# Performance work log

Hardware: AMD Instinct MI355X
Metric: run time of the kernel (lower is better)

Reference implementation:

```python
import jax, jax.numpy as jnp
import numpy as np

N_POINTS = 1_000_000
# Voigt index pairs (11,22,33,12,13,23)
_II = jnp.array([0, 1, 2, 0, 0, 1])
_JJ = jnp.array([0, 1, 2, 1, 2, 2])


def _P_of(F, c1, c2):
    """First Piola-Kirchhoff stress of compressible Neo-Hookean psi."""
    FinvT = jnp.linalg.inv(F).T
    I1 = jnp.trace(F.T @ F)
    J = jnp.linalg.det(F)
    Jm23 = jnp.power(J, -2.0 / 3.0)
    return 2.0 * c1 * Jm23 * (F - (I1 / 3.0) * FinvT) + 2.0 * c2 * (J - 1.0) * J * FinvT


def _per_point(F, c1, c2):
    I1 = jnp.trace(F.T @ F)
    J = jnp.linalg.det(F)
    Jm23 = jnp.power(J, -2.0 / 3.0)
    psi = c1 * (Jm23 * I1 - 3.0) + c2 * (J - 1.0) ** 2

    P = _P_of(F, c1, c2)                      # (3,3)
    P_F = jax.jacfwd(_P_of)(F, c1, c2)        # (3,3,3,3) = d P_ij / d F_kl

    Kirchhoff = P @ F.T                       # tau = P F^T
    Cauchy = Kirchhoff / J
    EYE = jnp.eye(3, dtype=F.dtype)

    # push-forward of the material tangent + geometric correction
    Stiff = jnp.einsum('iqks,jq,ls->ijkl', P_F, F, F)
    Stiff = Stiff + 0.5 * (
        jnp.einsum('ik,jl->ijkl', Kirchhoff, EYE)
        + jnp.einsum('il,jk->ijkl', Kirchhoff, EYE)
        + jnp.einsum('jk,il->ijkl', Kirchhoff, EYE)
        - jnp.einsum('jl,ik->ijkl', Kirchhoff, EYE)
    )

    Cauchy6 = Cauchy[_II, _JJ]                                            # (6,)
    DDSDDE = Stiff[_II[:, None], _JJ[:, None], _II[None, :], _JJ[None, :]] / J  # (6,6)
    return psi, Cauchy6, DDSDDE


def setup_inputs() -> dict:
    key = jax.random.key(0)
    k1, k2 = jax.random.split(key)
    # near-identity deformation gradients (positive det, small strain)
    noise = jax.random.normal(k1, (N_POINTS, 3, 3), dtype=jnp.float32)
    F_in = jnp.eye(3, dtype=jnp.float32)[None] + 0.05 * noise
    mat_par = 0.5 + jax.random.uniform(k2, (2,), dtype=jnp.float32)  # (c1, c2) > 0
    return {"F_in": F_in, "mat_par": mat_par}


def reference(F_in, mat_par):
    c1, c2 = mat_par[0], mat_par[1]
    psi, Cauchy6, DDSDDE = jax.vmap(_per_point, in_axes=(0, None, None))(F_in, c1, c2)
    return psi, Cauchy6, DDSDDE
```

## Files before the change

kernel.cpp:

```cpp
#include <hip/hip_runtime.h>

static constexpr int VII[6] = {0, 1, 2, 0, 0, 1};
static constexpr int VJJ[6] = {0, 1, 2, 1, 2, 2};

__device__ __forceinline__ void nh_compute(const float F[3][3], float c1, float c2,
                                           float& psi, float cau[6], float dd[36])
{
    const float J = F[0][0] * (F[1][1] * F[2][2] - F[1][2] * F[2][1])
                  - F[0][1] * (F[1][0] * F[2][2] - F[1][2] * F[2][0])
                  + F[0][2] * (F[1][0] * F[2][1] - F[1][1] * F[2][0]);

    float b[3][3];
#pragma unroll
    for (int r = 0; r < 3; ++r)
#pragma unroll
        for (int c = 0; c < 3; ++c) {
            if (c > r) continue;
            const float s = F[r][0] * F[c][0] + F[r][1] * F[c][1] + F[r][2] * F[c][2];
            b[r][c] = s;
            b[c][r] = s;
        }

    const float I1   = b[0][0] + b[1][1] + b[2][2];
    const float invJ = 1.0f / J;
    const float Jm23 = cbrtf(invJ * invJ);

    psi = c1 * (Jm23 * I1 - 3.0f) + c2 * (J - 1.0f) * (J - 1.0f);

    const float c1t  = 2.0f * c1 * Jm23;
    const float diag = 2.0f * c2 * (J - 1.0f) * J - c1t * (I1 * (1.0f / 3.0f));
    float tau[3][3];
#pragma unroll
    for (int r = 0; r < 3; ++r)
#pragma unroll
        for (int c = 0; c < 3; ++c)
            tau[r][c] = c1t * b[r][c] + (r == c ? diag : 0.0f);

#pragma unroll
    for (int a = 0; a < 6; ++a)
        cau[a] = tau[VII[a]][VJJ[a]] * invJ;

    const float gE  = 2.0f * c2 * (2.0f * J - 1.0f) * J;
    const float gF  = -2.0f * c2 * (J - 1.0f) * J;
    const float cA  = c1t * (2.0f * I1 * (1.0f / 9.0f));
    const float cB  = c1t * (I1 * (1.0f / 3.0f));
    const float m23 = -(2.0f / 3.0f) * c1t;

#pragma unroll
    for (int a = 0; a < 6; ++a) {
        const int i = VII[a], j = VJJ[a];
#pragma unroll
        for (int q = 0; q < 6; ++q) {
            const int k = VII[q], l = VJJ[q];
            float s = 0.0f;
            if (i == k) s += c1t * b[j][l];
            if (k == l) s += m23 * b[i][j];
            if (i == j) s += m23 * b[k][l];
            if (i == j && k == l) s += cA + gE;
            if (i == l && j == k) s += cB + gF;
            float g = 0.0f;
            if (j == l) g += tau[i][k];
            if (j == k) g += tau[i][l];
            if (i == l) g += tau[j][k];
            if (i == k) g -= tau[j][l];
            dd[6 * a + q] = (s + 0.5f * g) * invJ;
        }
    }
}

#define WPB 4
#define DPAD 37

__global__ __launch_bounds__(256) void nh3d_coal(
    const float* __restrict__ Fg, const float* __restrict__ mp,
    float* __restrict__ out, int N, int nWaves)
{
    __shared__ float sbuf[WPB][64 * DPAD];

    const int tid  = threadIdx.x;
    const int wave = tid >> 6;
    const int lane = tid & 63;
    const int waveIdx = blockIdx.x * WPB + wave;
    if (waveIdx >= nWaves) return;
    const int waveStart = waveIdx * 64;
    const int idx = waveStart + lane;

    const float c1 = mp[0];
    const float c2 = mp[1];

    float F[3][3];
    {
        const float* fp = Fg + (size_t)idx * 9;
#pragma unroll
        for (int r = 0; r < 3; ++r)
#pragma unroll
            for (int c = 0; c < 3; ++c)
                F[r][c] = fp[3 * r + c];
    }

    float psi, cau[6], dd[36];
    nh_compute(F, c1, c2, psi, cau, dd);

    out[idx] = psi;

    float* sw = sbuf[wave];

#pragma unroll
    for (int j = 0; j < 36; ++j)
        sw[lane * DPAD + j] = dd[j];

    float* dout = out + (size_t)7 * N + (size_t)waveStart * 36;
#pragma unroll
    for (int k = 0; k < 9; ++k) {
        const int g = k * 256 + lane * 4;
        const int p = g / 36;
        const int base = p * DPAD + (g - p * 36);
        const float4 v = make_float4(sw[base], sw[base + 1], sw[base + 2], sw[base + 3]);
        *reinterpret_cast<float4*>(dout + g) = v;
    }

#pragma unroll
    for (int j = 0; j < 6; ++j)
        sw[lane * 7 + j] = cau[j];

    float* cout_ = out + (size_t)N + (size_t)waveStart * 6;
#pragma unroll
    for (int k = 0; k < 3; ++k) {
        const int g = k * 128 + lane * 2;
        const int p = g / 6;
        const int base = p * 7 + (g - p * 6);
        *reinterpret_cast<float2*>(cout_ + g) = make_float2(sw[base], sw[base + 1]);
    }
}

__global__ __launch_bounds__(256) void nh3d_scatter(
    const float* __restrict__ Fg, const float* __restrict__ mp,
    float* __restrict__ out, int N, int start)
{
    const int idx = start + blockIdx.x * blockDim.x + threadIdx.x;
    if (idx >= N) return;

    const float c1 = mp[0];
    const float c2 = mp[1];

    float F[3][3];
    {
        const float* fp = Fg + (size_t)idx * 9;
#pragma unroll
        for (int r = 0; r < 3; ++r)
#pragma unroll
            for (int c = 0; c < 3; ++c)
                F[r][c] = fp[3 * r + c];
    }

    float psi, cau[6], dd[36];
    nh_compute(F, c1, c2, psi, cau, dd);

    out[idx] = psi;
    float* cout_ = out + (size_t)N + (size_t)idx * 6;
    float* dout  = out + (size_t)7 * N + (size_t)idx * 36;
#pragma unroll
    for (int a = 0; a < 6; ++a) cout_[a] = cau[a];
#pragma unroll
    for (int a = 0; a < 36; ++a) dout[a] = dd[a];
}

extern "C" void kernel_launch(void* const* d_in, const int* in_sizes, int n_in,
                              void* d_out, int out_size, void* d_ws, size_t ws_size,
                              hipStream_t stream) {
    const int N = in_sizes[0] / 9;
    const float* F_in    = (const float*)d_in[0];
    const float* mat_par = (const float*)d_in[1];
    float* out = (float*)d_out;

    if (N >= 64 && (N % 4) == 0) {
        const int nWaves = N / 64;
        const int grid = (nWaves + WPB - 1) / WPB;
        nh3d_coal<<<grid, 256, 0, stream>>>(F_in, mat_par, out, N, nWaves);
        const int tail = N - nWaves * 64;
        if (tail > 0) {
            nh3d_scatter<<<1, 64, 0, stream>>>(F_in, mat_par, out, N, nWaves * 64);
        }
    } else {
        const int grid = (N + 255) / 256;
        nh3d_scatter<<<grid, 256, 0, stream>>>(F_in, mat_par, out, N, 0);
    }
}
```

Before: 194.0 us.

## Stage input through LDS, use vector LDS layout, nontemporal stores, fast math

The F input is loaded with coalesced float4 reads into LDS per wave and then read back per lane, replacing strided 9-float loads. The output staging now uses an unpadded float4 LDS layout, writes go out as nontemporal vector stores, and the symmetric DDSDDE matrix is computed only for its upper triangle and mirrored. J^-2/3 and 1/J use hardware log/exp2/rcp intrinsics in the fast path. The unpadded float4 LDS layout may cause bank conflicts, and the approximate intrinsics slightly change numerics.

```diff
diff --git a/kernel.cpp b/kernel.cpp
--- a/kernel.cpp
+++ b/kernel.cpp
@@ -1,8 +1,14 @@
 #include <hip/hip_runtime.h>
+
+typedef float f32x4 __attribute__((ext_vector_type(4)));
+typedef float f32x2 __attribute__((ext_vector_type(2)));
+
+#define LDS_FENCE() asm volatile("" ::: "memory")
 
 static constexpr int VII[6] = {0, 1, 2, 0, 0, 1};
 static constexpr int VJJ[6] = {0, 1, 2, 1, 2, 2};
 
+template <bool FAST>
 __device__ __forceinline__ void nh_compute(const float F[3][3], float c1, float c2,
                                            float& psi, float cau[6], float dd[36])
 {
@@ -14,16 +20,21 @@
 #pragma unroll
     for (int r = 0; r < 3; ++r)
 #pragma unroll
-        for (int c = 0; c < 3; ++c) {
-            if (c > r) continue;
+        for (int c = 0; c <= r; ++c) {
             const float s = F[r][0] * F[c][0] + F[r][1] * F[c][1] + F[r][2] * F[c][2];
             b[r][c] = s;
             b[c][r] = s;
         }
 
-    const float I1   = b[0][0] + b[1][1] + b[2][2];
-    const float invJ = 1.0f / J;
-    const float Jm23 = cbrtf(invJ * invJ);
+    const float I1 = b[0][0] + b[1][1] + b[2][2];
+    float invJ, Jm23;
+    if (FAST) {
+        invJ = __builtin_amdgcn_rcpf(J);
+        Jm23 = __builtin_amdgcn_exp2f(-(2.0f / 3.0f) * __builtin_amdgcn_logf(J));
+    } else {
+        invJ = 1.0f / J;
+        Jm23 = cbrtf(invJ * invJ);
+    }
 
     psi = c1 * (Jm23 * I1 - 3.0f) + c2 * (J - 1.0f) * (J - 1.0f);
 
@@ -50,7 +61,7 @@
     for (int a = 0; a < 6; ++a) {
         const int i = VII[a], j = VJJ[a];
 #pragma unroll
-        for (int q = 0; q < 6; ++q) {
+        for (int q = a; q < 6; ++q) {
             const int k = VII[q], l = VJJ[q];
             float s = 0.0f;
             if (i == k) s += c1t * b[j][l];
@@ -63,19 +74,20 @@
             if (j == k) g += tau[i][l];
             if (i == l) g += tau[j][k];
             if (i == k) g -= tau[j][l];
-            dd[6 * a + q] = (s + 0.5f * g) * invJ;
+            const float v = (s + 0.5f * g) * invJ;
+            dd[6 * a + q] = v;
+            if (q != a) dd[6 * q + a] = v;
         }
     }
 }
 
 #define WPB 4
-#define DPAD 37
 
 __global__ __launch_bounds__(256) void nh3d_coal(
     const float* __restrict__ Fg, const float* __restrict__ mp,
     float* __restrict__ out, int N, int nWaves)
 {
-    __shared__ float sbuf[WPB][64 * DPAD];
+    __shared__ f32x4 sbuf[WPB][576];
 
     const int tid  = threadIdx.x;
     const int wave = tid >> 6;
@@ -83,53 +95,59 @@
     const int waveIdx = blockIdx.x * WPB + wave;
     if (waveIdx >= nWaves) return;
     const int waveStart = waveIdx * 64;
-    const int idx = waveStart + lane;
 
     const float c1 = mp[0];
     const float c2 = mp[1];
 
+    f32x4* sv = sbuf[wave];
+    const float* sf = reinterpret_cast<const float*>(sv);
+
+    {
+        const f32x4* gin = reinterpret_cast<const f32x4*>(Fg + (size_t)waveStart * 9);
+        sv[lane]      = gin[lane];
+        sv[64 + lane] = gin[64 + lane];
+        if (lane < 16) sv[128 + lane] = gin[128 + lane];
+    }
+    LDS_FENCE();
     float F[3][3];
+#pragma unroll
+    for (int r = 0; r < 3; ++r)
+#pragma unroll
+        for (int c = 0; c < 3; ++c)
+            F[r][c] = sf[lane * 9 + 3 * r + c];
+    LDS_FENCE();
+
+    float psi, cau[6], dd[36];
+    nh_compute<true>(F, c1, c2, psi, cau, dd);
+
+    __builtin_nontemporal_store(psi, out + waveStart + lane);
+
+#pragma unroll
+    for (int q = 0; q < 9; ++q) {
+        f32x4 v = {dd[4 * q], dd[4 * q + 1], dd[4 * q + 2], dd[4 * q + 3]};
+        sv[lane * 9 + q] = v;
+    }
+    LDS_FENCE();
+
+    f32x4* dout = reinterpret_cast<f32x4*>(out + (size_t)7 * N) + (size_t)waveStart * 9;
+#pragma unroll
+    for (int k = 0; k < 9; ++k)
+        __builtin_nontemporal_store(sv[k * 64 + lane], dout + k * 64 + lane);
+    LDS_FENCE();
+
     {
-        const float* fp = Fg + (size_t)idx * 9;
-#pragma unroll
-        for (int r = 0; r < 3; ++r)
-#pragma unroll
-            for (int c = 0; c < 3; ++c)
-                F[r][c] = fp[3 * r + c];
-    }
-
-    float psi, cau[6], dd[36];
-    nh_compute(F, c1, c2, psi, cau, dd);
-
-    out[idx] = psi;
-
-    float* sw = sbuf[wave];
-
-#pragma unroll
-    for (int j = 0; j < 36; ++j)
-        sw[lane * DPAD + j] = dd[j];
-
-    float* dout = out + (size_t)7 * N + (size_t)waveStart * 36;
-#pragma unroll
-    for (int k = 0; k < 9; ++k) {
-        const int g = k * 256 + lane * 4;
-        const int p = g / 36;
-        const int base = p * DPAD + (g - p * 36);
-        const float4 v = make_float4(sw[base], sw[base + 1], sw[base + 2], sw[base + 3]);
-        *reinterpret_cast<float4*>(dout + g) = v;
-    }
-
-#pragma unroll
-    for (int j = 0; j < 6; ++j)
-        sw[lane * 7 + j] = cau[j];
-
-    float* cout_ = out + (size_t)N + (size_t)waveStart * 6;
-#pragma unroll
-    for (int k = 0; k < 3; ++k) {
-        const int g = k * 128 + lane * 2;
-        const int p = g / 6;
-        const int base = p * 7 + (g - p * 6);
-        *reinterpret_cast<float2*>(cout_ + g) = make_float2(sw[base], sw[base + 1]);
+        f32x2* sv2 = reinterpret_cast<f32x2*>(sv);
+#pragma unroll
+        for (int t = 0; t < 3; ++t) {
+            f32x2 v = {cau[2 * t], cau[2 * t + 1]};
+            sv2[lane * 3 + t] = v;
+        }
+        LDS_FENCE();
+
+        f32x4* cout_ = reinterpret_cast<f32x4*>(out + (size_t)N) + (size_t)waveStart * 6 / 4;
+        __builtin_nontemporal_store(sv[lane], cout_ + lane);
+        if (lane < 32)
+            __builtin_nontemporal_store(sv[64 + lane], cout_ + 64 + lane);
     }
 }
 
@@ -154,7 +172,7 @@
     }
 
     float psi, cau[6], dd[36];
-    nh_compute(F, c1, c2, psi, cau, dd);
+    nh_compute<false>(F, c1, c2, psi, cau, dd);
 
     out[idx] = psi;
     float* cout_ = out + (size_t)N + (size_t)idx * 6;
@@ -177,10 +195,8 @@
         const int nWaves = N / 64;
         const int grid = (nWaves + WPB - 1) / WPB;
         nh3d_coal<<<grid, 256, 0, stream>>>(F_in, mat_par, out, N, nWaves);
-        const int tail = N - nWaves * 64;
-        if (tail > 0) {
+        if (N - nWaves * 64 > 0)
             nh3d_scatter<<<1, 64, 0, stream>>>(F_in, mat_par, out, N, nWaves * 64);
-        }
     } else {
         const int grid = (N + 255) / 256;
         nh3d_scatter<<<grid, 256, 0, stream>>>(F_in, mat_par, out, N, 0);
```

Result: slower. 198.7 us (+2.5%).
